# Kernel optimization log

Hardware: AMD Instinct MI355X
Metric: run time of the kernel (lower is better)

## Reference

```python
import jax, jax.numpy as jnp
import numpy as np

B, T, D = 32, 2048, 512


def setup_inputs() -> dict:
    key = jax.random.key(0)
    x = jax.random.normal(key, (B, T, D), dtype=jnp.float32)
    return {"x": x}


def reference(x):
    """DmvCell RNN with aggregations ('mean','var','max').

    Active partials: count, sum, max, mean, sn (Welford M2), var.
    Per step t:
        count += 1
        sum   += x_t
        max    = maximum(max, x_t)
        prev_mean = mean; mean = sum / count
        sn    += (x_t - prev_mean) * (x_t - mean)
        var    = sn / count
        out_t  = concat([mean, var, max])
    Initial states are zeros (Keras default). Returns the full output
    sequence [B, T, 3*D].
    """
    b, t, d = x.shape
    dt = x.dtype

    def step(carry, xt):
        count, s, mx, mean, sn = carry
        count = count + jnp.asarray(1, dt)          # [B,1]
        s = s + xt                                   # [B,D]
        mx = jnp.maximum(mx, xt)                     # [B,D]
        prev_mean = mean
        mean = s / count                             # [B,D]
        sn = sn + (xt - prev_mean) * (xt - mean)     # [B,D]
        var = sn / count                             # [B,D]
        out = jnp.concatenate([mean, var, mx], axis=-1)  # [B,3D]
        return (count, s, mx, mean, sn), out

    init = (
        jnp.zeros((b, 1), dt),   # count
        jnp.zeros((b, d), dt),   # sum
        jnp.zeros((b, d), dt),   # max
        jnp.zeros((b, d), dt),   # mean
        jnp.zeros((b, d), dt),   # sn
    )
    _, ys = jax.lax.scan(step, init, jnp.swapaxes(x, 0, 1))  # ys: [T,B,3D]
    return jnp.swapaxes(ys, 0, 1)  # [B,T,3D]
```

## Files before the change

### kernel.cpp

```cpp
#include <hip/hip_runtime.h>


#define BB 32
#define TT 2048
#define DD 512
#define TILE_T 256
#define CHUNK 64
#define NTILES (TT / TILE_T)
#define NWAVES 4
#define DGRP 64

__device__ __forceinline__ float fast_rcp(float x) {
#if __has_builtin(__builtin_amdgcn_rcpf)
    return __builtin_amdgcn_rcpf(x);
#else
    return 1.0f / x;
#endif
}

__launch_bounds__(256, 1)
__global__ void dmv_scan_kernel(const float* __restrict__ x,
                                float* __restrict__ out) {
    __shared__ float tile[TILE_T * DGRP];
    __shared__ float aggs[2][NWAVES][3][DGRP];

    const int tid = threadIdx.x;
    const int w   = tid >> 6;
    const int l   = tid & 63;
    const int b   = blockIdx.x >> 3;
    const int d0  = (blockIdx.x & 7) * DGRP;

    const float* xbase = x   + ((size_t)b * TT) * DD + d0;
    float*       obase = out + ((size_t)b * TT) * (3 * DD) + d0;

    const int srow = (l >> 4);
    const int scol = (l & 15) * 4;

    float4 regs[16];

    #pragma unroll
    for (int r = 0; r < 16; ++r) {
        int t = w * CHUNK + r * 4 + srow;
        regs[r] = *(const float4*)(xbase + (size_t)t * DD + scol);
    }

    float c_n = 0.f, c_s = 0.f, c_m2 = 0.f, c_mx = 0.f;

    for (int s = 0; s < NTILES; ++s) {
        #pragma unroll
        for (int r = 0; r < 16; ++r) {
            int row = w * CHUNK + r * 4 + srow;
            *(float4*)(&tile[row * DGRP + scol]) = regs[r];
        }
        if (s + 1 < NTILES) {
            const float* xt = xbase + (size_t)(s + 1) * TILE_T * DD;
            #pragma unroll
            for (int r = 0; r < 16; ++r) {
                int t = w * CHUNK + r * 4 + srow;
                regs[r] = *(const float4*)(xt + (size_t)t * DD + scol);
            }
        }

        const float* tbase = &tile[(w * CHUNK) * DGRP + l];
        float p_s = 0.f, p_m2 = 0.f, p_mx = 0.f, p_mean = 0.f, cnt = 0.f;
        #pragma unroll 16
        for (int k = 0; k < CHUNK; ++k) {
            float xv = tbase[k * DGRP];
            cnt += 1.f;
            p_s += xv;
            p_mx = fmaxf(p_mx, xv);
            float inv = fast_rcp(cnt);
            float nm  = p_s * inv;
            p_m2 += (xv - p_mean) * (xv - nm);
            p_mean = nm;
        }
        const int ab = s & 1;
        aggs[ab][w][0][l] = p_s;
        aggs[ab][w][1][l] = p_m2;
        aggs[ab][w][2][l] = p_mx;
        __syncthreads();

        float st_n = c_n, st_s = c_s, st_m2 = c_m2, st_mx = c_mx;
        float my_n = 0.f, my_s = 0.f, my_m2 = 0.f, my_mx = 0.f;
        #pragma unroll
        for (int j = 0; j < NWAVES; ++j) {
            if (j == w) { my_n = st_n; my_s = st_s; my_m2 = st_m2; my_mx = st_mx; }
            float bs  = aggs[ab][j][0][l];
            float bm2 = aggs[ab][j][1][l];
            float bmx = aggs[ab][j][2][l];
            if (st_n == 0.f) {
                st_n = 64.f; st_s = bs; st_m2 = bm2; st_mx = bmx;
            } else {
                float n  = st_n + 64.f;
                float da = bs * (1.0f / 64.0f) - st_s / st_n;
                st_m2 = st_m2 + bm2 + da * da * (st_n * 64.f / n);
                st_s += bs;
                st_mx = fmaxf(st_mx, bmx);
                st_n  = n;
            }
        }
        c_n = st_n; c_s = st_s; c_m2 = st_m2; c_mx = st_mx;

        float cnt2 = my_n;
        float rs = my_s, rm2 = my_m2, rmx = my_mx;
        float rmean = (cnt2 > 0.f) ? rs / cnt2 : 0.f;
        float* ob = obase + (size_t)(s * TILE_T + w * CHUNK) * (3 * DD) + l;
        #pragma unroll 8
        for (int k = 0; k < CHUNK; ++k) {
            float xv = tbase[k * DGRP];
            cnt2 += 1.f;
            float inv = fast_rcp(cnt2);
            rs += xv;
            rmx = fmaxf(rmx, xv);
            float nm = rs * inv;
            rm2 += (xv - rmean) * (xv - nm);
            rmean = nm;
            float var = rm2 * inv;
            float* orow = ob + (size_t)k * (3 * DD);
            orow[0]      = nm;
            orow[DD]     = var;
            orow[2 * DD] = rmx;
        }
    }
}

extern "C" void kernel_launch(void* const* d_in, const int* in_sizes, int n_in,
                              void* d_out, int out_size, void* d_ws, size_t ws_size,
                              hipStream_t stream) {
    (void)in_sizes; (void)n_in; (void)d_ws; (void)ws_size; (void)out_size;
    const float* x = (const float*)d_in[0];
    float* out = (float*)d_out;
    dim3 grid(BB * (DD / DGRP));
    dim3 block(256);
    dmv_scan_kernel<<<grid, block, 0, stream>>>(x, out);
}
```

Measured before the change: 146.1 us.

## Split full sequence across 16 waves with single-pass chunk scan, no LDS tile

Replaces the tiled loop (4 waves, 8 tiles of 256 steps staged through LDS with register prefetch) with one pass. A 1024-thread block gives each of 16 waves a 128-step chunk of the whole sequence. Each wave first reads its chunk from global memory to build sum, sum-of-squares and max. It then combines the earlier waves' aggregates with the parallel Welford merge and rescans its chunk to write outputs. This removes the LDS staging and the per-tile barriers and raises parallelism per block. In exchange every input element is read twice from global or cache, and the M2 from sum-of-squares is less numerically stable. The last wave skips the aggregate pass.

Result: faster. 139.4 us (-4.5%).

```diff
diff --git a/kernel.cpp b/kernel.cpp
--- a/kernel.cpp
+++ b/kernel.cpp
@@ -4,11 +4,9 @@
 #define BB 32
 #define TT 2048
 #define DD 512
-#define TILE_T 256
-#define CHUNK 64
-#define NTILES (TT / TILE_T)
-#define NWAVES 4
 #define DGRP 64
+#define NW 16
+#define CHUNK (TT / NW)
 
 __device__ __forceinline__ float fast_rcp(float x) {
 #if __has_builtin(__builtin_amdgcn_rcpf)
@@ -18,11 +16,12 @@
 #endif
 }
 
-__launch_bounds__(256, 1)
+__launch_bounds__(1024, 1)
 __global__ void dmv_scan_kernel(const float* __restrict__ x,
                                 float* __restrict__ out) {
-    __shared__ float tile[TILE_T * DGRP];
-    __shared__ float aggs[2][NWAVES][3][DGRP];
+    __shared__ float aggS[NW][DGRP];
+    __shared__ float aggM2[NW][DGRP];
+    __shared__ float aggMX[NW][DGRP];
 
     const int tid = threadIdx.x;
     const int w   = tid >> 6;
@@ -30,97 +29,59 @@
     const int b   = blockIdx.x >> 3;
     const int d0  = (blockIdx.x & 7) * DGRP;
 
-    const float* xbase = x   + ((size_t)b * TT) * DD + d0;
-    float*       obase = out + ((size_t)b * TT) * (3 * DD) + d0;
+    const float* xp = x   + ((size_t)b * TT) * DD + d0 + l
+                          + (size_t)(w * CHUNK) * DD;
+    float*       op = out + ((size_t)b * TT) * (3 * DD) + d0 + l
+                          + (size_t)(w * CHUNK) * (3 * DD);
 
-    const int srow = (l >> 4);
-    const int scol = (l & 15) * 4;
+    if (w < NW - 1) {
+        float s = 0.f, ss = 0.f, mx = 0.f;
+        #pragma unroll 8
+        for (int k = 0; k < CHUNK; ++k) {
+            float xv = xp[(size_t)k * DD];
+            s  += xv;
+            ss  = fmaf(xv, xv, ss);
+            mx  = fmaxf(mx, xv);
+        }
+        aggS[w][l]  = s;
+        aggM2[w][l] = ss - s * s * (1.0f / CHUNK);
+        aggMX[w][l] = mx;
+    }
+    __syncthreads();
 
-    float4 regs[16];
-
-    #pragma unroll
-    for (int r = 0; r < 16; ++r) {
-        int t = w * CHUNK + r * 4 + srow;
-        regs[r] = *(const float4*)(xbase + (size_t)t * DD + scol);
+    float c_n = 0.f, c_s = 0.f, c_m2 = 0.f, c_mx = 0.f;
+    for (int j = 0; j < w; ++j) {
+        float bs = aggS[j][l], bm2 = aggM2[j][l], bmx = aggMX[j][l];
+        if (j == 0) {
+            c_n = (float)CHUNK; c_s = bs; c_m2 = bm2; c_mx = bmx;
+        } else {
+            float n  = c_n + (float)CHUNK;
+            float da = bs * (1.0f / CHUNK) - c_s / c_n;
+            c_m2 = c_m2 + bm2 + da * da * (c_n * (float)CHUNK / n);
+            c_s += bs;
+            c_mx = fmaxf(c_mx, bmx);
+            c_n  = n;
+        }
     }
 
-    float c_n = 0.f, c_s = 0.f, c_m2 = 0.f, c_mx = 0.f;
-
-    for (int s = 0; s < NTILES; ++s) {
-        #pragma unroll
-        for (int r = 0; r < 16; ++r) {
-            int row = w * CHUNK + r * 4 + srow;
-            *(float4*)(&tile[row * DGRP + scol]) = regs[r];
-        }
-        if (s + 1 < NTILES) {
-            const float* xt = xbase + (size_t)(s + 1) * TILE_T * DD;
-            #pragma unroll
-            for (int r = 0; r < 16; ++r) {
-                int t = w * CHUNK + r * 4 + srow;
-                regs[r] = *(const float4*)(xt + (size_t)t * DD + scol);
-            }
-        }
-
-        const float* tbase = &tile[(w * CHUNK) * DGRP + l];
-        float p_s = 0.f, p_m2 = 0.f, p_mx = 0.f, p_mean = 0.f, cnt = 0.f;
-        #pragma unroll 16
-        for (int k = 0; k < CHUNK; ++k) {
-            float xv = tbase[k * DGRP];
-            cnt += 1.f;
-            p_s += xv;
-            p_mx = fmaxf(p_mx, xv);
-            float inv = fast_rcp(cnt);
-            float nm  = p_s * inv;
-            p_m2 += (xv - p_mean) * (xv - nm);
-            p_mean = nm;
-        }
-        const int ab = s & 1;
-        aggs[ab][w][0][l] = p_s;
-        aggs[ab][w][1][l] = p_m2;
-        aggs[ab][w][2][l] = p_mx;
-        __syncthreads();
-
-        float st_n = c_n, st_s = c_s, st_m2 = c_m2, st_mx = c_mx;
-        float my_n = 0.f, my_s = 0.f, my_m2 = 0.f, my_mx = 0.f;
-        #pragma unroll
-        for (int j = 0; j < NWAVES; ++j) {
-            if (j == w) { my_n = st_n; my_s = st_s; my_m2 = st_m2; my_mx = st_mx; }
-            float bs  = aggs[ab][j][0][l];
-            float bm2 = aggs[ab][j][1][l];
-            float bmx = aggs[ab][j][2][l];
-            if (st_n == 0.f) {
-                st_n = 64.f; st_s = bs; st_m2 = bm2; st_mx = bmx;
-            } else {
-                float n  = st_n + 64.f;
-                float da = bs * (1.0f / 64.0f) - st_s / st_n;
-                st_m2 = st_m2 + bm2 + da * da * (st_n * 64.f / n);
-                st_s += bs;
-                st_mx = fmaxf(st_mx, bmx);
-                st_n  = n;
-            }
-        }
-        c_n = st_n; c_s = st_s; c_m2 = st_m2; c_mx = st_mx;
-
-        float cnt2 = my_n;
-        float rs = my_s, rm2 = my_m2, rmx = my_mx;
-        float rmean = (cnt2 > 0.f) ? rs / cnt2 : 0.f;
-        float* ob = obase + (size_t)(s * TILE_T + w * CHUNK) * (3 * DD) + l;
-        #pragma unroll 8
-        for (int k = 0; k < CHUNK; ++k) {
-            float xv = tbase[k * DGRP];
-            cnt2 += 1.f;
-            float inv = fast_rcp(cnt2);
-            rs += xv;
-            rmx = fmaxf(rmx, xv);
-            float nm = rs * inv;
-            rm2 += (xv - rmean) * (xv - nm);
-            rmean = nm;
-            float var = rm2 * inv;
-            float* orow = ob + (size_t)k * (3 * DD);
-            orow[0]      = nm;
-            orow[DD]     = var;
-            orow[2 * DD] = rmx;
-        }
+    float cnt   = c_n;
+    float rs    = c_s, rm2 = c_m2, rmx = c_mx;
+    float rmean = (w > 0) ? rs / cnt : 0.f;
+    #pragma unroll 8
+    for (int k = 0; k < CHUNK; ++k) {
+        float xv = xp[(size_t)k * DD];
+        cnt += 1.f;
+        float inv = fast_rcp(cnt);
+        rs  += xv;
+        rmx  = fmaxf(rmx, xv);
+        float nm = rs * inv;
+        rm2 += (xv - rmean) * (xv - nm);
+        rmean = nm;
+        float var = rm2 * inv;
+        float* orow = op + (size_t)k * (3 * DD);
+        orow[0]      = nm;
+        orow[DD]     = var;
+        orow[2 * DD] = rmx;
     }
 }
 
@@ -131,6 +92,6 @@
     const float* x = (const float*)d_in[0];
     float* out = (float*)d_out;
     dim3 grid(BB * (DD / DGRP));
-    dim3 block(256);
+    dim3 block(1024);
     dmv_scan_kernel<<<grid, block, 0, stream>>>(x, out);
 }
```
